# Kernel tuning notes

Measured on AMD Instinct MI355X. Metric: run time of the kernel, lower is better.

Reference implementation:

```python
import jax, jax.numpy as jnp
import numpy as np

B, H, L, V = 128, 1024, 60, 50257


def setup_inputs() -> dict:
    key = jax.random.key(0)
    ks = jax.random.split(key, 14)
    s = 0.02
    f32 = jnp.float32
    return {
        "input": jax.random.randint(ks[0], (B,), 0, V),
        "hidden": jax.random.normal(ks[1], (1, B, H), f32),
        "encoder_outputs": jax.random.normal(ks[2], (B, L, H), f32),
        # learned parameters
        "emb": (jax.random.normal(ks[3], (V, H), f32) * s),
        "attn_W": (jax.random.normal(ks[4], (L, 2 * H), f32) * s),
        "attn_b": jnp.zeros((L,), f32),
        "comb_W": (jax.random.normal(ks[5], (H, 2 * H), f32) * s),
        "comb_b": jnp.zeros((H,), f32),
        "W_ih": (jax.random.normal(ks[6], (3 * H, H), f32) * s),
        "W_hh": (jax.random.normal(ks[7], (3 * H, H), f32) * s),
        "b_ih": jnp.zeros((3 * H,), f32),
        "b_hh": jnp.zeros((3 * H,), f32),
        "out_W": (jax.random.normal(ks[8], (V, H), f32) * s),
        "out_b": jnp.zeros((V,), f32),
    }


def reference(input, hidden, encoder_outputs, emb, attn_W, attn_b,
              comb_W, comb_b, W_ih, W_hh, b_ih, b_hh, out_W, out_b):
    # embedding lookup (dropout is identity in eval mode)
    embedded = emb[input]                      # [B, H]
    h = hidden[0]                              # [B, H]

    # Bahdanau-style attention over fixed max_length positions
    attn_logits = jnp.concatenate([embedded, h], axis=1) @ attn_W.T + attn_b  # [B, L]
    attn_weights = jax.nn.softmax(attn_logits, axis=1)                        # [B, L]
    attn_applied = jnp.einsum('bl,blh->bh', attn_weights, encoder_outputs)    # [B, H]

    # combine + relu
    x = jnp.concatenate([embedded, attn_applied], axis=1) @ comb_W.T + comb_b  # [B, H]
    x = jax.nn.relu(x)

    # single GRU step (PyTorch gate order: r, z, n)
    gi = x @ W_ih.T + b_ih                     # [B, 3H]
    gh = h @ W_hh.T + b_hh                     # [B, 3H]
    i_r, i_z, i_n = jnp.split(gi, 3, axis=1)
    h_r, h_z, h_n = jnp.split(gh, 3, axis=1)
    r = jax.nn.sigmoid(i_r + h_r)
    z = jax.nn.sigmoid(i_z + h_z)
    n = jnp.tanh(i_n + r * h_n)
    h_new = (1.0 - z) * n + z * h              # [B, H]

    # output projection + log_softmax over vocab
    logp = jax.nn.log_softmax(h_new @ out_W.T + out_b, axis=1)  # [B, V]
    return logp, h_new[None], attn_weights
```

## Files before the change

kernel.cpp:

```cpp
#include <hip/hip_runtime.h>
#include <hip/hip_bf16.h>

#define B_ 128
#define H_ 1024
#define L_ 60
#define V_ 50257

typedef __attribute__((ext_vector_type(8))) short bf16x8;
typedef __attribute__((ext_vector_type(4))) float f32x4;

__device__ __forceinline__ unsigned short f2bf(float f) {
  union { __hip_bfloat16 h; unsigned short u; } v;
  v.h = __float2bfloat16(f);
  return v.u;
}

__device__ __forceinline__ bf16x8 cvt8(float4 a, float4 b) {
  union { bf16x8 v; __hip_bfloat16 h[8]; } u;
  u.h[0] = __float2bfloat16(a.x); u.h[1] = __float2bfloat16(a.y);
  u.h[2] = __float2bfloat16(a.z); u.h[3] = __float2bfloat16(a.w);
  u.h[4] = __float2bfloat16(b.x); u.h[5] = __float2bfloat16(b.y);
  u.h[6] = __float2bfloat16(b.z); u.h[7] = __float2bfloat16(b.w);
  return u.v;
}

__device__ __forceinline__ void gl_lds16(const void* g, void* l) {
  __builtin_amdgcn_global_load_lds(
      (const __attribute__((address_space(1))) unsigned int*)g,
      (__attribute__((address_space(3))) unsigned int*)l, 16, 0, 0);
}

#define SBAR()   __builtin_amdgcn_s_barrier()
#define SCHED0() __builtin_amdgcn_sched_barrier(0)
__device__ __forceinline__ void vwait6() { asm volatile("s_waitcnt vmcnt(6)" ::: "memory"); }
__device__ __forceinline__ void vwait0() { asm volatile("s_waitcnt vmcnt(0)" ::: "memory"); }

__device__ __forceinline__ size_t packIdx(int b, int k) {
  int s = k >> 5;
  int bm = b >> 4;
  int lane = (b & 15) | (((k >> 3) & 3) << 4);
  return ((size_t)((s * 8 + bm) * 64 + lane) << 3) | (size_t)(k & 7);
}

__global__ __launch_bounds__(256) void k_front(
    const int* __restrict__ input, const float* __restrict__ hidden,
    const float* __restrict__ emb, const float* __restrict__ attn_W,
    const float* __restrict__ attn_b, unsigned short* __restrict__ aXa,
    unsigned short* __restrict__ aH, float* __restrict__ lbuf)
{
  int bx = blockIdx.x;
  if (bx < 512) {
    int idx = bx * 256 + threadIdx.x;
    int b = idx >> 10, j = idx & (H_ - 1);
    float e = emb[(size_t)input[b] * H_ + j];
    float h = hidden[idx];
    size_t p = packIdx(b, j);
    aXa[p] = f2bf(e);
    aH[p]  = f2bf(h);
  } else {
    int t = threadIdx.x, wv = t >> 6, lane = t & 63;
    int task = (bx - 512) * 4 + wv;
    int b = task / L_, l = task - b * L_;
    const float* erow = emb + (size_t)input[b] * H_;
    const float* hrow = hidden + (size_t)b * H_;
    const float* wr = attn_W + (size_t)l * (2 * H_);
    float acc = 0.f;
    #pragma unroll 4
    for (int i = 0; i < 16; ++i) {
      int m = lane + i * 64;
      acc += erow[m] * wr[m] + hrow[m] * wr[H_ + m];
    }
    #pragma unroll
    for (int off = 32; off; off >>= 1) acc += __shfl_xor(acc, off);
    if (lane == 0) lbuf[b * 64 + l] = acc + attn_b[l];
  }
}

__global__ __launch_bounds__(256) void k_appsm(
    const float* __restrict__ enc, const float* __restrict__ lbuf,
    float* __restrict__ attnw, unsigned short* __restrict__ aXa)
{
  __shared__ float sWt[64];
  int b = blockIdx.x, q = blockIdx.y, t = threadIdx.x;
  if (t < 64) {
    float v = (t < L_) ? lbuf[b * 64 + t] : -1e30f;
    float m = v;
    #pragma unroll
    for (int off = 32; off; off >>= 1) m = fmaxf(m, __shfl_xor(m, off));
    float e = (t < L_) ? __expf(v - m) : 0.f;
    float s = e;
    #pragma unroll
    for (int off = 32; off; off >>= 1) s += __shfl_xor(s, off);
    float w = e / s;
    sWt[t] = w;
    if (q == 0 && t < L_) attnw[b * L_ + t] = w;
  }
  __syncthreads();
  int col = q * 256 + t;
  const float* eb = enc + (size_t)b * L_ * H_ + col;
  float acc = 0.f;
  #pragma unroll 4
  for (int l = 0; l < L_; ++l) acc += sWt[l] * eb[(size_t)l * H_];
  aXa[packIdx(b, H_ + col)] = f2bf(acc);
}

__global__ __launch_bounds__(256, 5) void k_gemm(
    const unsigned short* __restrict__ Apk, const unsigned short* __restrict__ Apk2,
    const float* __restrict__ Wt, const float* __restrict__ Wt2,
    const float* __restrict__ bias, float* __restrict__ Cdir,
    float* __restrict__ Cpart, float* __restrict__ Cpart2,
    float* __restrict__ pms, int K, int N, int nchunks, int halfY, int nblkx)
{
  __shared__ __align__(16) float bufW0[64 * 32];
  __shared__ __align__(16) float bufW1[64 * 32];
  int t = threadIdx.x, wv = t >> 6, lane = t & 63;
  int y = blockIdx.y;
  const unsigned short* A = Apk;
  const float* W = Wt;
  float* CP = Cpart;
  int sidx = y;
  if (halfY && y >= halfY) { A = Apk2; W = Wt2; CP = Cpart2; sidx = y - halfY; }
  int chunk0 = sidx * nchunks;
  int n0 = blockIdx.x * 64;
  int ch = wv & 1;
  int bm0 = (wv >> 1) * 4;
  int srow8 = lane >> 3;
  int sch = lane & 7;
  int g = lane >> 4;

  f32x4 acc[4][2];
  #pragma unroll
  for (int i = 0; i < 4; ++i)
    #pragma unroll
    for (int j = 0; j < 2; ++j) acc[i][j] = (f32x4){0.f, 0.f, 0.f, 0.f};

  auto SW = [&](int kc, float* buf) {
    #pragma unroll
    for (int i = 0; i < 2; ++i) {
      int r = wv * 16 + i * 8 + srow8;
      int gcol = n0 + r; gcol = (gcol < N) ? gcol : (N - 1);
      int c = sch ^ (r & 7);
      const float* src = W + (size_t)gcol * K + (size_t)kc * 32 + c * 4;
      gl_lds16(src, buf + (wv * 16 + i * 8) * 32);
    }
  };
  const bf16x8* apg = (const bf16x8*)A;
  auto LA = [&](int kc, bf16x8* x) {
    #pragma unroll
    for (int j = 0; j < 4; ++j)
      x[j] = apg[((size_t)kc * 8 + bm0 + j) * 64 + lane];
  };
  auto COMP = [&](const float* bw, const bf16x8* a) {
    #pragma unroll
    for (int nci = 0; nci < 2; ++nci) {
      int rr = (ch * 2 + nci) * 16 + (lane & 15);
      int c0 = (g * 2) ^ (rr & 7);
      int c1 = (g * 2 + 1) ^ (rr & 7);
      float4 w0 = *(const float4*)&bw[rr * 32 + c0 * 4];
      float4 w1 = *(const float4*)&bw[rr * 32 + c1 * 4];
      bf16x8 bfr = cvt8(w0, w1);
      #pragma unroll
      for (int j = 0; j < 4; ++j)
        acc[j][nci] = __builtin_amdgcn_mfma_f32_16x16x32_bf16(a[j], bfr, acc[j][nci], 0, 0, 0);
    }
  };

  bf16x8 aA[4], aB[4];
  SW(chunk0, bufW0);     LA(chunk0, aA);
  SW(chunk0 + 1, bufW1); LA(chunk0 + 1, aB);
  vwait6(); SCHED0(); SBAR();

  for (int kk = 0; kk < nchunks; kk += 2) {
    COMP(bufW0, aA);
    SCHED0(); SBAR();
    if (kk + 2 < nchunks) { SW(chunk0 + kk + 2, bufW0); LA(chunk0 + kk + 2, aA); vwait6(); }
    else vwait0();
    SCHED0(); SBAR();
    COMP(bufW1, aB);
    if (kk + 2 < nchunks) {
      SCHED0(); SBAR();
      if (kk + 3 < nchunks) { SW(chunk0 + kk + 3, bufW1); LA(chunk0 + kk + 3, aB); vwait6(); }
      else vwait0();
      SCHED0(); SBAR();
    }
  }

  int cols[2]; float bv[2];
  #pragma unroll
  for (int nci = 0; nci < 2; ++nci) {
    int c = n0 + (ch * 2 + nci) * 16 + (lane & 15);
    cols[nci] = c;
    bv[nci] = (bias && c < N) ? bias[c] : 0.f;
  }
  int rb = (lane >> 4) * 4;
  if (CP) {
    float* dst = CP + (size_t)sidx * B_ * N;
    #pragma unroll
    for (int bm = 0; bm < 4; ++bm)
      #pragma unroll
      for (int r = 0; r < 4; ++r) {
        int row = (bm0 + bm) * 16 + rb + r;
        #pragma unroll
        for (int nci = 0; nci < 2; ++nci)
          if (cols[nci] < N) dst[(size_t)row * N + cols[nci]] = acc[bm][nci][r];
      }
  } else {
    #pragma unroll
    for (int bm = 0; bm < 4; ++bm)
      #pragma unroll
      for (int r = 0; r < 4; ++r) {
        int row = (bm0 + bm) * 16 + rb + r;
        #pragma unroll
        for (int nci = 0; nci < 2; ++nci)
          if (cols[nci] < N) Cdir[(size_t)row * N + cols[nci]] = acc[bm][nci][r] + bv[nci];
      }
    if (pms) {
      #pragma unroll
      for (int bm = 0; bm < 4; ++bm)
        #pragma unroll
        for (int r = 0; r < 4; ++r) {
          int row = (bm0 + bm) * 16 + rb + r;
          float m = -1e30f;
          #pragma unroll
          for (int nci = 0; nci < 2; ++nci)
            if (cols[nci] < N) m = fmaxf(m, acc[bm][nci][r] + bv[nci]);
          #pragma unroll
          for (int off = 8; off; off >>= 1) m = fmaxf(m, __shfl_xor(m, off));
          float e = 0.f;
          #pragma unroll
          for (int nci = 0; nci < 2; ++nci)
            if (cols[nci] < N) e += __expf(acc[bm][nci][r] + bv[nci] - m);
          #pragma unroll
          for (int off = 8; off; off >>= 1) e += __shfl_xor(e, off);
          if ((lane & 15) == 0) {
            size_t o = ((size_t)row * (2 * nblkx) + blockIdx.x * 2 + ch) * 2;
            pms[o] = m; pms[o + 1] = e;
          }
        }
    }
  }
}

__global__ __launch_bounds__(256) void k_reduce_comb(
    const float* __restrict__ parts, const float* __restrict__ bias,
    unsigned short* __restrict__ aX)
{
  int idx = blockIdx.x * 256 + threadIdx.x;
  int b = idx >> 10, j = idx & (H_ - 1);
  float s = bias[j];
  #pragma unroll
  for (int p = 0; p < 16; ++p) s += parts[(size_t)p * B_ * H_ + idx];
  s = fmaxf(s, 0.f);
  aX[packIdx(b, j)] = f2bf(s);
}

__global__ __launch_bounds__(256) void k_gate(
    const float* __restrict__ giP, const float* __restrict__ ghP,
    const float* __restrict__ b_ih, const float* __restrict__ b_hh,
    const float* __restrict__ hidden, float* __restrict__ hnew,
    unsigned short* __restrict__ aHn)
{
  int idx = blockIdx.x * 256 + threadIdx.x;
  int b = idx >> 10, j = idx & (H_ - 1);
  size_t base = (size_t)b * 3 * H_;
  float ir = b_ih[j], iz = b_ih[H_ + j], in_ = b_ih[2 * H_ + j];
  float hr = b_hh[j], hz = b_hh[H_ + j], hn = b_hh[2 * H_ + j];
  #pragma unroll
  for (int p = 0; p < 4; ++p) {
    const float* gi = giP + (size_t)p * B_ * 3 * H_ + base;
    const float* gh = ghP + (size_t)p * B_ * 3 * H_ + base;
    ir += gi[j]; iz += gi[H_ + j]; in_ += gi[2 * H_ + j];
    hr += gh[j]; hz += gh[H_ + j]; hn += gh[2 * H_ + j];
  }
  float r = 1.f / (1.f + __expf(-(ir + hr)));
  float z = 1.f / (1.f + __expf(-(iz + hz)));
  float n = tanhf(in_ + r * hn);
  float h = hidden[idx];
  float hv = (1.f - z) * n + z * h;
  hnew[idx] = hv;
  aHn[packIdx(b, j)] = f2bf(hv);
}

#define SL_ 6283
__global__ __launch_bounds__(256) void k_lsub(
    float* __restrict__ logits, const float* __restrict__ pms, int nblk2)
{
  __shared__ float sm[4], ss[4], sc;
  int b = blockIdx.x, sl = blockIdx.y, t = threadIdx.x;
  float M = -1e30f, S = 0.f;
  for (int i = t; i < nblk2; i += 256) {
    float m = pms[((size_t)b * nblk2 + i) * 2];
    float s = pms[((size_t)b * nblk2 + i) * 2 + 1];
    float nm = fmaxf(M, m);
    S = S * __expf(M - nm) + s * __expf(m - nm);
    M = nm;
  }
  #pragma unroll
  for (int off = 32; off; off >>= 1) {
    float m2 = __shfl_xor(M, off), s2 = __shfl_xor(S, off);
    float nm = fmaxf(M, m2);
    S = S * __expf(M - nm) + s2 * __expf(m2 - nm);
    M = nm;
  }
  if ((t & 63) == 0) { sm[t >> 6] = M; ss[t >> 6] = S; }
  __syncthreads();
  if (t == 0) {
    float Mf = sm[0], Sf = ss[0];
    #pragma unroll
    for (int i = 1; i < 4; ++i) {
      float nm = fmaxf(Mf, sm[i]);
      Sf = Sf * __expf(Mf - nm) + ss[i] * __expf(sm[i] - nm);
      Mf = nm;
    }
    sc = Mf + logf(Sf);
  }
  __syncthreads();
  float c = sc;
  int v0 = sl * SL_;
  int v1 = v0 + SL_; if (v1 > V_) v1 = V_;
  float* row = logits + (size_t)b * V_;
  for (int v = v0 + t; v < v1; v += 256) row[v] -= c;
}

extern "C" void kernel_launch(void* const* d_in, const int* in_sizes, int n_in,
                              void* d_out, int out_size, void* d_ws, size_t ws_size,
                              hipStream_t stream)
{
  const int*   input  = (const int*)d_in[0];
  const float* hidden = (const float*)d_in[1];
  const float* enc    = (const float*)d_in[2];
  const float* emb    = (const float*)d_in[3];
  const float* attn_W = (const float*)d_in[4];
  const float* attn_b = (const float*)d_in[5];
  const float* comb_W = (const float*)d_in[6];
  const float* comb_b = (const float*)d_in[7];
  const float* W_ih   = (const float*)d_in[8];
  const float* W_hh   = (const float*)d_in[9];
  const float* b_ih   = (const float*)d_in[10];
  const float* b_hh   = (const float*)d_in[11];
  const float* out_W  = (const float*)d_in[12];
  const float* out_b  = (const float*)d_in[13];

  float* out    = (float*)d_out;
  float* logits = out;
  float* hnew   = out + (size_t)B_ * V_;
  float* attnw  = hnew + (size_t)B_ * H_;

  const int NBLK = (V_ + 63) / 64;
  char* ws = (char*)d_ws;
  unsigned short* aXa = (unsigned short*)(ws);
  unsigned short* aH  = (unsigned short*)(ws + 524288);
  unsigned short* aX  = (unsigned short*)(ws + 786432);
  unsigned short* aHn = (unsigned short*)(ws + 1048576);
  float* lbuf  = (float*)(ws + 1310720);
  float* pms   = (float*)(ws + 1343488);
  float* combP = (float*)(ws + 4194304);
  float* giP   = (float*)(ws + 4194304);
  float* ghP   = (float*)(ws + 4194304 + 6291456);

  k_front<<<512 + (B_ * L_) / 4, 256, 0, stream>>>(input, hidden, emb, attn_W, attn_b,
                                                   aXa, aH, lbuf);
  k_appsm<<<dim3(B_, 4), 256, 0, stream>>>(enc, lbuf, attnw, aXa);
  k_gemm<<<dim3(16, 16), 256, 0, stream>>>(aXa, nullptr, comb_W, nullptr, nullptr,
                                           nullptr, combP, nullptr, nullptr,
                                           2 * H_, H_, 4, 0, 0);
  k_reduce_comb<<<(B_ * H_) / 256, 256, 0, stream>>>(combP, comb_b, aX);
  k_gemm<<<dim3(48, 8), 256, 0, stream>>>(aX, aH, W_ih, W_hh, nullptr,
                                          nullptr, giP, ghP, nullptr,
                                          H_, 3 * H_, 8, 4, 0);
  k_gate<<<(B_ * H_) / 256, 256, 0, stream>>>(giP, ghP, b_ih, b_hh, hidden, hnew, aHn);
  k_gemm<<<dim3(NBLK, 1), 256, 0, stream>>>(aHn, nullptr, out_W, nullptr, out_b,
                                            logits, nullptr, nullptr, pms,
                                            H_, V_, 32, 0, NBLK);
  k_lsub<<<dim3(B_, 8), 256, 0, stream>>>(logits, pms, 2 * NBLK);
}
```

Measured before the change: 130.2 us.

## Convert weight tiles to bf16 in registers before staging to LDS

Weight chunks are now loaded from global memory into registers, converted once to bf16, and written to a half-size bf16 LDS tile with a new swizzle. This replaces direct global-to-LDS fp32 loads that each wave then re-read and re-converted, so conversion and LDS traffic are no longer duplicated. It also drops one barrier per chunk and lowers the occupancy hint from 5 to 4 blocks per CU. In exchange, prefetch depth shrinks to one chunk in registers and the conversion sits on the critical path before each barrier, which may expose more of the global load latency in this bandwidth-heavy GEMM.

```diff
diff --git a/kernel.cpp b/kernel.cpp
--- a/kernel.cpp
+++ b/kernel.cpp
@@ -24,16 +24,9 @@
   return u.v;
 }
 
-__device__ __forceinline__ void gl_lds16(const void* g, void* l) {
-  __builtin_amdgcn_global_load_lds(
-      (const __attribute__((address_space(1))) unsigned int*)g,
-      (__attribute__((address_space(3))) unsigned int*)l, 16, 0, 0);
-}
-
 #define SBAR()   __builtin_amdgcn_s_barrier()
 #define SCHED0() __builtin_amdgcn_sched_barrier(0)
-__device__ __forceinline__ void vwait6() { asm volatile("s_waitcnt vmcnt(6)" ::: "memory"); }
-__device__ __forceinline__ void vwait0() { asm volatile("s_waitcnt vmcnt(0)" ::: "memory"); }
+__device__ __forceinline__ void lwait0() { asm volatile("s_waitcnt lgkmcnt(0)" ::: "memory"); }
 
 __device__ __forceinline__ size_t packIdx(int b, int k) {
   int s = k >> 5;
@@ -104,15 +97,15 @@
   aXa[packIdx(b, H_ + col)] = f2bf(acc);
 }
 
-__global__ __launch_bounds__(256, 5) void k_gemm(
+__global__ __launch_bounds__(256, 4) void k_gemm(
     const unsigned short* __restrict__ Apk, const unsigned short* __restrict__ Apk2,
     const float* __restrict__ Wt, const float* __restrict__ Wt2,
     const float* __restrict__ bias, float* __restrict__ Cdir,
     float* __restrict__ Cpart, float* __restrict__ Cpart2,
     float* __restrict__ pms, int K, int N, int nchunks, int halfY, int nblkx)
 {
-  __shared__ __align__(16) float bufW0[64 * 32];
-  __shared__ __align__(16) float bufW1[64 * 32];
+  __shared__ __align__(16) unsigned short bufW0[64 * 32];
+  __shared__ __align__(16) unsigned short bufW1[64 * 32];
   int t = threadIdx.x, wv = t >> 6, lane = t & 63;
   int y = blockIdx.y;
   const unsigned short* A = Apk;
@@ -124,25 +117,26 @@
   int n0 = blockIdx.x * 64;
   int ch = wv & 1;
   int bm0 = (wv >> 1) * 4;
-  int srow8 = lane >> 3;
-  int sch = lane & 7;
   int g = lane >> 4;
 
+  int sr  = wv * 16 + (lane >> 2);
+  int sj  = lane & 3;
+  int ssl = sj ^ ((sr >> 1) & 3);
+  int sgcol = n0 + sr; sgcol = (sgcol < N) ? sgcol : (N - 1);
+  const float* wsrc = W + (size_t)sgcol * K + sj * 8;
+  unsigned short* wdst0 = &bufW0[sr * 32 + ssl * 8];
+  unsigned short* wdst1 = &bufW1[sr * 32 + ssl * 8];
+
   f32x4 acc[4][2];
   #pragma unroll
   for (int i = 0; i < 4; ++i)
     #pragma unroll
     for (int j = 0; j < 2; ++j) acc[i][j] = (f32x4){0.f, 0.f, 0.f, 0.f};
 
-  auto SW = [&](int kc, float* buf) {
-    #pragma unroll
-    for (int i = 0; i < 2; ++i) {
-      int r = wv * 16 + i * 8 + srow8;
-      int gcol = n0 + r; gcol = (gcol < N) ? gcol : (N - 1);
-      int c = sch ^ (r & 7);
-      const float* src = W + (size_t)gcol * K + (size_t)kc * 32 + c * 4;
-      gl_lds16(src, buf + (wv * 16 + i * 8) * 32);
-    }
+  auto GW = [&](int kc, float4& lo, float4& hi) {
+    const float* p = wsrc + (size_t)kc * 32;
+    lo = *(const float4*)p;
+    hi = *(const float4*)(p + 4);
   };
   const bf16x8* apg = (const bf16x8*)A;
   auto LA = [&](int kc, bf16x8* x) {
@@ -150,39 +144,32 @@
     for (int j = 0; j < 4; ++j)
       x[j] = apg[((size_t)kc * 8 + bm0 + j) * 64 + lane];
   };
-  auto COMP = [&](const float* bw, const bf16x8* a) {
+  auto COMP = [&](const unsigned short* buf, const bf16x8* a) {
     #pragma unroll
     for (int nci = 0; nci < 2; ++nci) {
       int rr = (ch * 2 + nci) * 16 + (lane & 15);
-      int c0 = (g * 2) ^ (rr & 7);
-      int c1 = (g * 2 + 1) ^ (rr & 7);
-      float4 w0 = *(const float4*)&bw[rr * 32 + c0 * 4];
-      float4 w1 = *(const float4*)&bw[rr * 32 + c1 * 4];
-      bf16x8 bfr = cvt8(w0, w1);
+      int s = g ^ ((rr >> 1) & 3);
+      bf16x8 bfr = *(const bf16x8*)&buf[rr * 32 + s * 8];
       #pragma unroll
       for (int j = 0; j < 4; ++j)
         acc[j][nci] = __builtin_amdgcn_mfma_f32_16x16x32_bf16(a[j], bfr, acc[j][nci], 0, 0, 0);
     }
   };
 
+  float4 lo0, hi0, lo1, hi1;
   bf16x8 aA[4], aB[4];
-  SW(chunk0, bufW0);     LA(chunk0, aA);
-  SW(chunk0 + 1, bufW1); LA(chunk0 + 1, aB);
-  vwait6(); SCHED0(); SBAR();
+  GW(chunk0, lo0, hi0); LA(chunk0, aA);
 
   for (int kk = 0; kk < nchunks; kk += 2) {
+    if (kk + 1 < nchunks) { GW(chunk0 + kk + 1, lo1, hi1); LA(chunk0 + kk + 1, aB); }
+    *(bf16x8*)wdst0 = cvt8(lo0, hi0);
+    lwait0(); SCHED0(); SBAR(); SCHED0();
     COMP(bufW0, aA);
-    SCHED0(); SBAR();
-    if (kk + 2 < nchunks) { SW(chunk0 + kk + 2, bufW0); LA(chunk0 + kk + 2, aA); vwait6(); }
-    else vwait0();
-    SCHED0(); SBAR();
+    if (kk + 1 >= nchunks) break;
+    if (kk + 2 < nchunks) { GW(chunk0 + kk + 2, lo0, hi0); LA(chunk0 + kk + 2, aA); }
+    *(bf16x8*)wdst1 = cvt8(lo1, hi1);
+    lwait0(); SCHED0(); SBAR(); SCHED0();
     COMP(bufW1, aB);
-    if (kk + 2 < nchunks) {
-      SCHED0(); SBAR();
-      if (kk + 3 < nchunks) { SW(chunk0 + kk + 3, bufW1); LA(chunk0 + kk + 3, aB); vwait6(); }
-      else vwait0();
-      SCHED0(); SBAR();
-    }
   }
 
   int cols[2]; float bv[2];
```

New measurement: 131.9 us. No clear change (+1.3%).
